# Performance work log

Hardware: AMD Instinct MI355X
Metric: run time of the kernel (lower is better)

## Reference

```python
import jax, jax.numpy as jnp
import numpy as np

B, C, HZ, WZ, HX, WX = 128, 256, 8, 8, 32, 32
NC = HZ * WZ              # correlation channels = num_channel = 64
TC = max(8, NC // 32)     # CoordAttention bottleneck channels = 8
EPS = 1e-5


def setup_inputs() -> dict:
    key = jax.random.key(0)
    ks = jax.random.split(key, 8)
    z = jax.random.normal(ks[0], (B, C, HZ, WZ), dtype=jnp.float32)
    x = jax.random.normal(ks[1], (B, C, HX, WX), dtype=jnp.float32)
    # 1x1 conv weights stored as [out, in]
    conv1_w = jax.random.normal(ks[2], (TC, NC), dtype=jnp.float32) * (1.0 / np.sqrt(NC))
    conv1_b = jnp.zeros((TC,), dtype=jnp.float32)
    bn_gamma = jnp.ones((TC,), dtype=jnp.float32)
    bn_beta = jnp.zeros((TC,), dtype=jnp.float32)
    conv2_w = jax.random.normal(ks[3], (NC, TC), dtype=jnp.float32) * (1.0 / np.sqrt(TC))
    conv2_b = jnp.zeros((NC,), dtype=jnp.float32)
    conv3_w = jax.random.normal(ks[4], (NC, TC), dtype=jnp.float32) * (1.0 / np.sqrt(TC))
    conv3_b = jnp.zeros((NC,), dtype=jnp.float32)
    return dict(z=z, x=x, conv1_w=conv1_w, conv1_b=conv1_b, bn_gamma=bn_gamma,
                bn_beta=bn_beta, conv2_w=conv2_w, conv2_b=conv2_b,
                conv3_w=conv3_w, conv3_b=conv3_b)


def _h_swish(v):
    return v * jnp.clip(v + 3.0, 0.0, 6.0) / 6.0  # x * relu6(x+3)/6


def reference(z, x, conv1_w, conv1_b, bn_gamma, bn_beta, conv2_w, conv2_b, conv3_w, conv3_b):
    b, c, H, W = x.shape
    # pixel-wise correlation (per-sample loop == batched matmul): [b, Hz*Wz, H, W]
    corr = jnp.einsum('bck,bcn->bkn', z.reshape(b, c, -1), x.reshape(b, c, -1))
    corr = corr.reshape(b, -1, H, W)
    # CoordAttention
    x_h = corr.mean(axis=3)                       # pool over W -> [b, NC, H]
    x_w = corr.mean(axis=2)                       # pool over H -> [b, NC, W]
    x_cat = jnp.concatenate([x_h, x_w], axis=2)   # [b, NC, H+W]
    y = jnp.einsum('oc,bcl->bol', conv1_w, x_cat) + conv1_b[None, :, None]
    # BatchNorm2d (training-mode batch statistics, biased variance)
    mu = y.mean(axis=(0, 2), keepdims=True)
    var = y.var(axis=(0, 2), keepdims=True)
    y = (y - mu) * jax.lax.rsqrt(var + EPS) * bn_gamma[None, :, None] + bn_beta[None, :, None]
    y = _h_swish(y)
    yh, yw = y[:, :, :H], y[:, :, H:]
    out_h = jax.nn.sigmoid(jnp.einsum('oc,bcl->bol', conv2_w, yh) + conv2_b[None, :, None])  # [b, NC, H]
    out_w = jax.nn.sigmoid(jnp.einsum('oc,bcl->bol', conv3_w, yw) + conv3_b[None, :, None])  # [b, NC, W]
    return corr * out_w[:, :, None, :] * out_h[:, :, :, None]
```

## Files before the change

### kernel.cpp

```cpp
#include <hip/hip_runtime.h>
#include <hip/hip_bf16.h>
#include <math.h>

#define B_   128
#define C_   256
#define K_   64
#define N_   1024
#define H_   32
#define W_   32
#define TC_  8
#define L_   64
#define EPS_ 1e-5f

typedef __attribute__((address_space(3))) void       as3_void;
typedef const __attribute__((address_space(1))) void as1_void;

__device__ __forceinline__ void gload16(const float* g, float* lds) {
    __builtin_amdgcn_global_load_lds((as1_void*)g, (as3_void*)lds, 16, 0, 0);
}

__global__ __launch_bounds__(256) __attribute__((amdgpu_waves_per_eu(1, 2)))
void kA_corr(const float* __restrict__ z,
             const float* __restrict__ x,
             float* __restrict__ corr)
{
    __shared__ float zs[2][32][64];
    __shared__ float xs[2][32][256];

    const int nt   = blockIdx.x;
    const int b    = blockIdx.y;
    const int tid  = threadIdx.x;
    const int wv   = tid >> 6;
    const int lane = tid & 63;
    const int tk   = tid >> 5;
    const int tn   = tid & 31;

    const float* zb = z + (size_t)b * C_ * K_;
    const float* xb = x + (size_t)b * C_ * N_ + nt * 256;

    const int sl = lane ^ ((lane >> 4) & 1);
    const int s0 = (2 * tn)     ^ (((2 * tn)     >> 4) & 1);
    const int s1 = (2 * tn + 1) ^ (((2 * tn + 1) >> 4) & 1);

    const float* zg = zb + (lane >> 4) * K_ + (lane & 15) * 4;
    const float* xg = xb + sl * 4;

    float acc[8][8] = {};

    auto stage = [&](int buf, int cs2) {
        const int cc = cs2 * 32;
        #pragma unroll
        for (int q = 0; q < 10; ++q) {
            const int ch = wv + 4 * q;
            if (ch < 8) {
                gload16(zg + (size_t)(cc + ch * 4) * K_, &zs[buf][ch * 4][0]);
            } else {
                gload16(xg + (size_t)(cc + ch - 8) * N_, &xs[buf][ch - 8][0]);
            }
        }
    };

    stage(0, 0);

    for (int cs = 0; cs < 8; ++cs) {
        const int cur = cs & 1;
        if (cs < 7) {
            stage(cur ^ 1, cs + 1);
            asm volatile("s_waitcnt vmcnt(10)" ::: "memory");
        } else {
            asm volatile("s_waitcnt vmcnt(0)" ::: "memory");
        }
        __builtin_amdgcn_s_barrier();
        asm volatile("" ::: "memory");

        #pragma unroll 4
        for (int c = 0; c < 32; ++c) {
            float4 z0 = *(float4*)&zs[cur][c][tk * 8];
            float4 z1 = *(float4*)&zs[cur][c][tk * 8 + 4];
            float4 x0 = *(float4*)&xs[cur][c][s0 * 4];
            float4 x1 = *(float4*)&xs[cur][c][s1 * 4];
            float za[8] = {z0.x, z0.y, z0.z, z0.w, z1.x, z1.y, z1.z, z1.w};
            float xa[8] = {x0.x, x0.y, x0.z, x0.w, x1.x, x1.y, x1.z, x1.w};
            #pragma unroll
            for (int i = 0; i < 8; ++i)
                #pragma unroll
                for (int j = 0; j < 8; ++j)
                    acc[i][j] = fmaf(za[i], xa[j], acc[i][j]);
        }

        asm volatile("" ::: "memory");
        __builtin_amdgcn_s_barrier();
    }

    float* cb = corr + (size_t)b * K_ * N_ + nt * 256;
    #pragma unroll
    for (int i = 0; i < 8; ++i) {
        float4 lo = make_float4(acc[i][0], acc[i][1], acc[i][2], acc[i][3]);
        float4 hi = make_float4(acc[i][4], acc[i][5], acc[i][6], acc[i][7]);
        *(float4*)&cb[(size_t)(tk * 8 + i) * N_ + tn * 8]     = lo;
        *(float4*)&cb[(size_t)(tk * 8 + i) * N_ + tn * 8 + 4] = hi;
    }
}

__global__ __launch_bounds__(256) void kB_pool(const float* __restrict__ corr,
                                               const float* __restrict__ w1,
                                               const float* __restrict__ b1,
                                               float* __restrict__ ypre,
                                               float* __restrict__ psum)
{
    __shared__ float rs[4][1024];
    __shared__ float xc[64][64];
    __shared__ float w1s[TC_ * 64];
    __shared__ float ys[TC_ * 64];

    const int b   = blockIdx.x;
    const int tid = threadIdx.x;
    const float* cb = corr + (size_t)b * K_ * N_;

    if (tid < 128) *(float4*)&w1s[tid * 4] = *(const float4*)&w1[tid * 4];

    for (int pass = 0; pass < 16; ++pass) {
        #pragma unroll
        for (int i = 0; i < 4; ++i) {
            int q   = tid + i * 256;
            int kcl = q >> 8;
            int off = (q & 255) * 4;
            *(float4*)&rs[kcl][off] =
                *(const float4*)&cb[(size_t)(pass * 4 + kcl) * N_ + off];
        }
        __syncthreads();

        if (tid < 128) {
            int kcl = tid >> 5, h = tid & 31;
            float s = 0.f;
            #pragma unroll
            for (int m = 0; m < 8; ++m) {
                float4 v = *(float4*)&rs[kcl][h * 32 + (((m + h) & 7) << 2)];
                s += v.x + v.y + v.z + v.w;
            }
            xc[pass * 4 + kcl][h] = s * (1.f / 32.f);
        } else {
            int kcl = (tid - 128) >> 5, w = (tid - 128) & 31;
            float s = 0.f;
            #pragma unroll
            for (int h2 = 0; h2 < 32; ++h2) s += rs[kcl][h2 * 32 + w];
            xc[pass * 4 + kcl][32 + w] = s * (1.f / 32.f);
        }
        __syncthreads();
    }

    const int o0 = tid >> 6;
    const int l  = tid & 63;
    float y0 = 0.f, y1 = 0.f;
    #pragma unroll 8
    for (int k = 0; k < 64; ++k) {
        float xv = xc[k][l];
        y0 = fmaf(w1s[o0 * 64 + k],       xv, y0);
        y1 = fmaf(w1s[(o0 + 4) * 64 + k], xv, y1);
    }
    y0 += b1[o0];
    y1 += b1[o0 + 4];
    ypre[((size_t)b * TC_ + o0)     * L_ + l] = y0;
    ypre[((size_t)b * TC_ + o0 + 4) * L_ + l] = y1;
    ys[o0 * L_ + l]       = y0;
    ys[(o0 + 4) * L_ + l] = y1;
    __syncthreads();

    if (tid < TC_) {
        float s = 0.f, sq = 0.f;
        #pragma unroll
        for (int m = 0; m < 16; ++m) {
            float4 v = *(float4*)&ys[tid * 64 + m * 4];
            s  += v.x + v.y + v.z + v.w;
            sq += v.x * v.x + v.y * v.y + v.z * v.z + v.w * v.w;
        }
        psum[b * 16 + tid]       = s;
        psum[b * 16 + 8 + tid]   = sq;
    }
}

__global__ __launch_bounds__(256) void kD_gate(const float* __restrict__ ypre,
                                               const float* __restrict__ psum,
                                               const float* __restrict__ gamma,
                                               const float* __restrict__ beta,
                                               const float* __restrict__ w2,
                                               const float* __restrict__ b2,
                                               const float* __restrict__ w3,
                                               const float* __restrict__ b3,
                                               float* __restrict__ outh,
                                               float* __restrict__ outw)
{
    __shared__ float sred[16][17];
    __shared__ float stats[16];
    __shared__ float yn[TC_ * L_];
    __shared__ float w2s[K_ * TC_];
    __shared__ float w3s[K_ * TC_];
    __shared__ float b2s[K_], b3s[K_];

    const int b   = blockIdx.x;
    const int tid = threadIdx.x;

    {
        float p = 0.f;
        #pragma unroll
        for (int m = 0; m < 8; ++m) p += psum[tid + 256 * m];
        sred[tid & 15][tid >> 4] = p;
    }
    __syncthreads();
    if (tid < 16) {
        float s = 0.f;
        #pragma unroll
        for (int c = 0; c < 16; ++c) s += sred[tid][c];
        stats[tid] = s;
    }
    __syncthreads();

    const float inv_n = 1.f / (float)(B_ * L_);
    #pragma unroll
    for (int r = 0; r < 2; ++r) {
        int idx = tid + r * 256;
        int o   = idx >> 6;
        float mu  = stats[o] * inv_n;
        float var = stats[8 + o] * inv_n - mu * mu;
        float v = ypre[(size_t)b * TC_ * L_ + idx];
        v = (v - mu) * (1.f / sqrtf(var + EPS_)) * gamma[o] + beta[o];
        v = v * fminf(fmaxf(v + 3.f, 0.f), 6.f) * (1.f / 6.f);
        yn[idx] = v;
    }
    if (tid < 128)      *(float4*)&w2s[tid * 4]         = *(const float4*)&w2[tid * 4];
    else                *(float4*)&w3s[(tid - 128) * 4] = *(const float4*)&w3[(tid - 128) * 4];
    if (tid < 64)       b2s[tid]      = b2[tid];
    else if (tid < 128) b3s[tid - 64] = b3[tid - 64];
    __syncthreads();

    #pragma unroll
    for (int r = 0; r < 16; ++r) {
        int idx   = tid + r * 256;
        int which = idx >> 11;
        int o     = (idx >> 5) & 63;
        int p     = idx & 31;
        const float* wsm = which ? w3s : w2s;
        const float* bsm = which ? b3s : b2s;
        float s = bsm[o];
        #pragma unroll
        for (int tt = 0; tt < TC_; ++tt)
            s = fmaf(wsm[o * TC_ + tt], yn[tt * L_ + which * H_ + p], s);
        s = 1.f / (1.f + __expf(-s));
        float* dst = which ? outw : outh;
        dst[((size_t)b * K_ + o) * H_ + p] = s;
    }
}

__global__ __launch_bounds__(256) void kE_final(float* __restrict__ out,
                                                const float* __restrict__ outh,
                                                const float* __restrict__ outw)
{
    int idx = blockIdx.x * 256 + threadIdx.x;
    int w4 = idx & 7;
    int h  = (idx >> 3) & 31;
    int bk = idx >> 8;
    float4 c4 = ((const float4*)out)[idx];
    float  oh = outh[bk * H_ + h];
    float4 ow = *(const float4*)&outw[bk * H_ + w4 * 4];
    c4.x *= ow.x * oh;
    c4.y *= ow.y * oh;
    c4.z *= ow.z * oh;
    c4.w *= ow.w * oh;
    ((float4*)out)[idx] = c4;
}

extern "C" void kernel_launch(void* const* d_in, const int* in_sizes, int n_in,
                              void* d_out, int out_size, void* d_ws, size_t ws_size,
                              hipStream_t stream)
{
    const float* z     = (const float*)d_in[0];
    const float* x     = (const float*)d_in[1];
    const float* w1    = (const float*)d_in[2];
    const float* b1    = (const float*)d_in[3];
    const float* gamma = (const float*)d_in[4];
    const float* beta  = (const float*)d_in[5];
    const float* w2    = (const float*)d_in[6];
    const float* b2    = (const float*)d_in[7];
    const float* w3    = (const float*)d_in[8];
    const float* b3    = (const float*)d_in[9];
    float* out = (float*)d_out;
    float* ws  = (float*)d_ws;

    float* ypre = ws;
    float* psum = ws + 65536;
    float* outh = ws + 67584;
    float* outw = ws + 329728;

    kA_corr <<<dim3(4, B_), 256, 0, stream>>>(z, x, out);
    kB_pool <<<B_,          256, 0, stream>>>(out, w1, b1, ypre, psum);
    kD_gate <<<B_,          256, 0, stream>>>(ypre, psum, gamma, beta,
                                              w2, b2, w3, b3, outh, outw);
    kE_final<<<(B_ * K_ * N_) / (256 * 4), 256, 0, stream>>>(out, outh, outw);
}
```

Before: 266.8 us.

## Halve correlation block threads and double per-thread register tile to 16x8

The correlation GEMM kernel now runs with 128 threads per block, each computing a 16x8 output tile instead of 8x8, with channel stages shrunk from 32 to 16 and the LDS swizzle adjusted. The aim is more register-level reuse of LDS reads per FMA and less LDS traffic. In exchange, register pressure rises, fewer waves are available to hide global memory latency, and the number of barrier-separated stages doubles.

```diff
diff --git a/kernel.cpp b/kernel.cpp
--- a/kernel.cpp
+++ b/kernel.cpp
@@ -19,13 +19,13 @@
     __builtin_amdgcn_global_load_lds((as1_void*)g, (as3_void*)lds, 16, 0, 0);
 }
 
-__global__ __launch_bounds__(256) __attribute__((amdgpu_waves_per_eu(1, 2)))
+__global__ __launch_bounds__(128) __attribute__((amdgpu_waves_per_eu(1, 2)))
 void kA_corr(const float* __restrict__ z,
              const float* __restrict__ x,
              float* __restrict__ corr)
 {
-    __shared__ float zs[2][32][64];
-    __shared__ float xs[2][32][256];
+    __shared__ float zs[2][16][64];
+    __shared__ float xs[2][16][256];
 
     const int nt   = blockIdx.x;
     const int b    = blockIdx.y;
@@ -34,37 +34,39 @@
     const int lane = tid & 63;
     const int tk   = tid >> 5;
     const int tn   = tid & 31;
+    const int k0   = tk * 16;
 
     const float* zb = z + (size_t)b * C_ * K_;
     const float* xb = x + (size_t)b * C_ * N_ + nt * 256;
 
-    const int sl = lane ^ ((lane >> 4) & 1);
-    const int s0 = (2 * tn)     ^ (((2 * tn)     >> 4) & 1);
-    const int s1 = (2 * tn + 1) ^ (((2 * tn + 1) >> 4) & 1);
-
-    const float* zg = zb + (lane >> 4) * K_ + (lane & 15) * 4;
-    const float* xg = xb + sl * 4;
-
-    float acc[8][8] = {};
+    const int slx = lane ^ ((lane >> 3) & 7);
+    const int s0  = (2 * tn)     ^ (((2 * tn)     >> 3) & 7);
+    const int s1  = (2 * tn + 1) ^ (((2 * tn + 1) >> 3) & 7);
+
+    const int zlr = lane >> 4;
+    const int zlc = (lane & 15) * 4;
+
+    float acc[16][8] = {};
 
     auto stage = [&](int buf, int cs2) {
-        const int cc = cs2 * 32;
-        #pragma unroll
-        for (int q = 0; q < 10; ++q) {
-            const int ch = wv + 4 * q;
-            if (ch < 8) {
-                gload16(zg + (size_t)(cc + ch * 4) * K_, &zs[buf][ch * 4][0]);
-            } else {
-                gload16(xg + (size_t)(cc + ch - 8) * N_, &xs[buf][ch - 8][0]);
-            }
+        const int cc = cs2 * 16;
+        #pragma unroll
+        for (int i = 0; i < 2; ++i) {
+            const int rg = (wv * 2 + i) * 4;
+            gload16(zb + (size_t)(cc + rg + zlr) * K_ + zlc, &zs[buf][rg][0]);
+        }
+        #pragma unroll
+        for (int i = 0; i < 8; ++i) {
+            const int r = wv * 8 + i;
+            gload16(xb + (size_t)(cc + r) * N_ + slx * 4, &xs[buf][r][0]);
         }
     };
 
     stage(0, 0);
 
-    for (int cs = 0; cs < 8; ++cs) {
+    for (int cs = 0; cs < 16; ++cs) {
         const int cur = cs & 1;
-        if (cs < 7) {
+        if (cs < 15) {
             stage(cur ^ 1, cs + 1);
             asm volatile("s_waitcnt vmcnt(10)" ::: "memory");
         } else {
@@ -74,15 +76,18 @@
         asm volatile("" ::: "memory");
 
         #pragma unroll 4
-        for (int c = 0; c < 32; ++c) {
-            float4 z0 = *(float4*)&zs[cur][c][tk * 8];
-            float4 z1 = *(float4*)&zs[cur][c][tk * 8 + 4];
+        for (int c = 0; c < 16; ++c) {
+            float4 z0 = *(float4*)&zs[cur][c][k0];
+            float4 z1 = *(float4*)&zs[cur][c][k0 + 4];
+            float4 z2 = *(float4*)&zs[cur][c][k0 + 8];
+            float4 z3 = *(float4*)&zs[cur][c][k0 + 12];
             float4 x0 = *(float4*)&xs[cur][c][s0 * 4];
             float4 x1 = *(float4*)&xs[cur][c][s1 * 4];
-            float za[8] = {z0.x, z0.y, z0.z, z0.w, z1.x, z1.y, z1.z, z1.w};
-            float xa[8] = {x0.x, x0.y, x0.z, x0.w, x1.x, x1.y, x1.z, x1.w};
+            float za[16] = {z0.x, z0.y, z0.z, z0.w, z1.x, z1.y, z1.z, z1.w,
+                            z2.x, z2.y, z2.z, z2.w, z3.x, z3.y, z3.z, z3.w};
+            float xa[8]  = {x0.x, x0.y, x0.z, x0.w, x1.x, x1.y, x1.z, x1.w};
             #pragma unroll
-            for (int i = 0; i < 8; ++i)
+            for (int i = 0; i < 16; ++i)
                 #pragma unroll
                 for (int j = 0; j < 8; ++j)
                     acc[i][j] = fmaf(za[i], xa[j], acc[i][j]);
@@ -92,13 +97,13 @@
         __builtin_amdgcn_s_barrier();
     }
 
-    float* cb = corr + (size_t)b * K_ * N_ + nt * 256;
+    float* cb = corr + (size_t)b * K_ * N_ + nt * 256 + tn * 8;
     #pragma unroll
-    for (int i = 0; i < 8; ++i) {
+    for (int i = 0; i < 16; ++i) {
         float4 lo = make_float4(acc[i][0], acc[i][1], acc[i][2], acc[i][3]);
         float4 hi = make_float4(acc[i][4], acc[i][5], acc[i][6], acc[i][7]);
-        *(float4*)&cb[(size_t)(tk * 8 + i) * N_ + tn * 8]     = lo;
-        *(float4*)&cb[(size_t)(tk * 8 + i) * N_ + tn * 8 + 4] = hi;
+        *(float4*)&cb[(size_t)(k0 + i) * N_]     = lo;
+        *(float4*)&cb[(size_t)(k0 + i) * N_ + 4] = hi;
     }
 }
 
@@ -291,7 +296,7 @@
     float* outh = ws + 67584;
     float* outw = ws + 329728;
 
-    kA_corr <<<dim3(4, B_), 256, 0, stream>>>(z, x, out);
+    kA_corr <<<dim3(4, B_), 128, 0, stream>>>(z, x, out);
     kB_pool <<<B_,          256, 0, stream>>>(out, w1, b1, ypre, psum);
     kD_gate <<<B_,          256, 0, stream>>>(ypre, psum, gamma, beta,
                                               w2, b2, w3, b3, outh, outw);
```

New measurement: 296.9 us. 1.11x slower.
